# Kernel tuning notes

Measured on AMD Instinct MI355X. Metric: run time of the kernel, lower is better.

Reference implementation:

```python
import jax, jax.numpy as jnp
import numpy as np

B, S, D, H, W = 8, 2048, 128, 8, 64
INT_HEADS = 8          # hardcoded in SpatioTemporalLayer1
EPS_COS = 1e-8
EPS_LN = 1e-5


def _mha(q_in, k_in, v_in, in_w, in_b, out_w, out_b, nh, mask=None):
    # q_in/k_in/v_in: (batch, len, d); torch nn.MultiheadAttention math (eval, no dropout)
    b, lq, d = q_in.shape
    hd = d // nh
    q = (q_in @ in_w[:d].T + in_b[:d]).reshape(b, lq, nh, hd)
    k = (k_in @ in_w[d:2 * d].T + in_b[d:2 * d]).reshape(b, k_in.shape[1], nh, hd)
    v = (v_in @ in_w[2 * d:].T + in_b[2 * d:]).reshape(b, v_in.shape[1], nh, hd)
    scores = jnp.einsum('bihd,bjhd->bhij', q, k) / jnp.sqrt(jnp.asarray(hd, q_in.dtype))
    if mask is not None:
        scores = scores + mask
    attn = jax.nn.softmax(scores, axis=-1)
    out = jnp.einsum('bhij,bjhd->bihd', attn, v).reshape(b, lq, d)
    return out @ out_w.T + out_b


def _layernorm(x, g, b):
    mu = x.mean(-1, keepdims=True)
    var = ((x - mu) ** 2).mean(-1, keepdims=True)
    return (x - mu) * jax.lax.rsqrt(var + EPS_LN) * g + b


def _cos_normalize(e):
    n = jnp.maximum(jnp.linalg.norm(e, axis=-1, keepdims=True), EPS_COS)
    return e / n


def _forward(x, spatial_info, temporal_info,
             lw_in_w, lw_in_b, lw_out_w, lw_out_b,
             spat_w, spat_b, temp_w, temp_b,
             int_in_w, int_in_b, int_out_w, int_out_b,
             ffn_w1, ffn_b1, ffn_w2, ffn_b2,
             ln1_g, ln1_b, ln2_g, ln2_b):
    b, s, d = x.shape
    # --- local window attention (S % W == 0 here, so no padding path) ---
    nw = s // W
    xw = x.reshape(b * nw, W, d)
    causal = jnp.triu(jnp.full((W, W), -jnp.inf, x.dtype), k=1)
    attn = _mha(xw, xw, xw, lw_in_w, lw_in_b, lw_out_w, lw_out_b, H, causal).reshape(b, s, d)
    x = _layernorm(attn + x, ln1_g, ln1_b)
    # --- FFN (torch nn.GELU default = exact erf) ---
    h = jax.nn.gelu(x @ ffn_w1.T + ffn_b1, approximate=False)
    x = _layernorm(h @ ffn_w2.T + ffn_b2 + x, ln2_g, ln2_b)
    # --- spatio-temporal interaction ---
    se = spatial_info @ spat_w.T + spat_b
    te = temporal_info @ temp_w.T + temp_b
    sn = _cos_normalize(se)
    tn = _cos_normalize(te)
    ss = jnp.einsum('bid,bjd->bij', sn, sn)   # (B,S,S) spatial cosine sim
    ts = jnp.einsum('bid,bjd->bij', tn, tn)   # (B,S,S) temporal cosine sim
    # interaction MHA is batch_first=False: it treats (B,S,D) as (len=B, batch=S, d).
    # Equivalent batch-first call on swapped axes (faithful to the torch source).
    inter = jnp.swapaxes(
        _mha(jnp.swapaxes(se, 0, 1), jnp.swapaxes(te, 0, 1), jnp.swapaxes(te, 0, 1),
             int_in_w, int_in_b, int_out_w, int_out_b, INT_HEADS), 0, 1)
    # similarity[b,i,j,d] = ss[b,i,j]*ts[b,i,j]*inter[b,i,d]; mean over j factorizes:
    sim = (ss * ts).mean(axis=2)              # (B,S)
    return x + sim[..., None] * inter


def setup_inputs() -> dict:
    key = jax.random.key(0)
    ks = jax.random.split(key, 24)
    sc = 0.02
    inp = {
        'x': jax.random.normal(ks[0], (B, S, D), jnp.float32),
        'spatial_info': jax.random.normal(ks[1], (B, S, D), jnp.float32),
        'temporal_info': jax.random.normal(ks[2], (B, S, D), jnp.float32),
        'lw_in_w': jax.random.normal(ks[3], (3 * D, D), jnp.float32) * sc,
        'lw_in_b': jnp.zeros((3 * D,), jnp.float32),
        'lw_out_w': jax.random.normal(ks[4], (D, D), jnp.float32) * sc,
        'lw_out_b': jnp.zeros((D,), jnp.float32),
        'spat_w': jax.random.normal(ks[5], (D, D), jnp.float32) * sc,
        'spat_b': jnp.zeros((D,), jnp.float32),
        'temp_w': jax.random.normal(ks[6], (D, D), jnp.float32) * sc,
        'temp_b': jnp.zeros((D,), jnp.float32),
        'int_in_w': jax.random.normal(ks[7], (3 * D, D), jnp.float32) * sc,
        'int_in_b': jnp.zeros((3 * D,), jnp.float32),
        'int_out_w': jax.random.normal(ks[8], (D, D), jnp.float32) * sc,
        'int_out_b': jnp.zeros((D,), jnp.float32),
        'ffn_w1': jax.random.normal(ks[9], (4 * D, D), jnp.float32) * sc,
        'ffn_b1': jnp.zeros((4 * D,), jnp.float32),
        'ffn_w2': jax.random.normal(ks[10], (D, 4 * D), jnp.float32) * sc,
        'ffn_b2': jnp.zeros((D,), jnp.float32),
        'ln1_g': jnp.ones((D,), jnp.float32),
        'ln1_b': jnp.zeros((D,), jnp.float32),
        'ln2_g': jnp.ones((D,), jnp.float32),
        'ln2_b': jnp.zeros((D,), jnp.float32),
    }
    return inp


def reference(x, spatial_info, temporal_info,
              lw_in_w, lw_in_b, lw_out_w, lw_out_b,
              spat_w, spat_b, temp_w, temp_b,
              int_in_w, int_in_b, int_out_w, int_out_b,
              ffn_w1, ffn_b1, ffn_w2, ffn_b2,
              ln1_g, ln1_b, ln2_g, ln2_b):
    return _forward(x, spatial_info, temporal_info,
                    lw_in_w, lw_in_b, lw_out_w, lw_out_b,
                    spat_w, spat_b, temp_w, temp_b,
                    int_in_w, int_in_b, int_out_w, int_out_b,
                    ffn_w1, ffn_b1, ffn_w2, ffn_b2,
                    ln1_g, ln1_b, ln2_g, ln2_b)
```

## Files before the change

### kernel.cpp

```cpp
#include <hip/hip_runtime.h>
#include <math.h>

#define BB 8
#define SS 2048
#define NTOK (BB * SS)
#define ATB_SPLIT 16

using bf16x8 = __attribute__((ext_vector_type(8))) short;
using f32x4  = __attribute__((ext_vector_type(4))) float;

__device__ __forceinline__ float gelu_tanh(float x) {
    float y = 0.7978845608f * (x + 0.044715f * x * x * x);
    float e = __expf(2.0f * y);
    float t = 1.0f - 2.0f / (e + 1.0f);
    return 0.5f * x * (1.0f + t);
}
__device__ __forceinline__ unsigned short f2b(float f) {
    unsigned int u = __float_as_uint(f);
    u += 0x7FFFu + ((u >> 16) & 1u);
    return (unsigned short)(u >> 16);
}
__device__ __forceinline__ float b2f(unsigned short u) {
    return __uint_as_float((unsigned int)u << 16);
}
__device__ __forceinline__ bf16x8 ldg_f32_b8(const float* p) {
    float4 f0 = *(const float4*)p, f1 = *(const float4*)(p + 4);
    union { ushort4 u[2]; bf16x8 v; } r;
    r.u[0] = (ushort4){f2b(f0.x), f2b(f0.y), f2b(f0.z), f2b(f0.w)};
    r.u[1] = (ushort4){f2b(f1.x), f2b(f1.y), f2b(f1.z), f2b(f1.w)};
    return r.v;
}

__global__ __launch_bounds__(256) void phase1(
    const float* __restrict__ x,
    const float* __restrict__ lw_in_w, const float* __restrict__ b_in,
    const float* __restrict__ lw_out_w, const float* __restrict__ b_out,
    const float* __restrict__ lng, const float* __restrict__ lnb,
    float* __restrict__ x1, unsigned short* __restrict__ x1b,
    const float* __restrict__ ffn_w1, const float* __restrict__ ffn_w2,
    unsigned short* __restrict__ Wb,
    const float* __restrict__ spatial, const float* __restrict__ temporal,
    const float* __restrict__ spat_w, const float* __restrict__ temp_w,
    const float* __restrict__ bsp, const float* __restrict__ btp,
    unsigned short* __restrict__ snb, unsigned short* __restrict__ tnb,
    unsigned short* __restrict__ seb, unsigned short* __restrict__ teb)
{
    __shared__ unsigned short Qs[64 * 136];
    __shared__ unsigned short Ks[64 * 136];
    __shared__ unsigned short Vt[128 * 72];
    __shared__ unsigned short Pb[4][32 * 72];
    __shared__ float red[2][64][2];
    const int tid = threadIdx.x;
    const int wv = tid >> 6, lane = tid & 63, ln = lane & 15, q = lane >> 4;

    if (blockIdx.x >= 768) {
        const int idx2 = blockIdx.x - 768;
        const int y = idx2 >> 8;
        const int m0 = (idx2 & 255) * 64;
        const float* Af = y ? temporal : spatial;
        const float* Wf = y ? temp_w : spat_w;
        const float* bias = y ? btp : bsp;
        unsigned short* nb = y ? tnb : snb;
        unsigned short* raw = y ? teb : seb;
        const int wm = (wv >> 1) * 32, wn = (wv & 1) * 64;

        f32x4 acc[2][4] = {};
        #pragma unroll
        for (int kf = 0; kf < 4; ++kf) {
            bf16x8 a[2], b[4];
            #pragma unroll
            for (int fm = 0; fm < 2; ++fm)
                a[fm] = ldg_f32_b8(Af + (size_t)(m0 + wm + fm * 16 + ln) * 128 + kf * 32 + q * 8);
            #pragma unroll
            for (int fn = 0; fn < 4; ++fn)
                b[fn] = ldg_f32_b8(Wf + (size_t)(wn + fn * 16 + ln) * 128 + kf * 32 + q * 8);
            #pragma unroll
            for (int fm = 0; fm < 2; ++fm)
                #pragma unroll
                for (int fn = 0; fn < 4; ++fn)
                    acc[fm][fn] = __builtin_amdgcn_mfma_f32_16x16x32_bf16(a[fm], b[fn], acc[fm][fn], 0, 0, 0);
        }
        #pragma unroll
        for (int fm = 0; fm < 2; ++fm)
            #pragma unroll
            for (int r = 0; r < 4; ++r) {
                int rl = wm + fm * 16 + q * 4 + r;
                float s2 = 0.0f;
                #pragma unroll
                for (int fn = 0; fn < 4; ++fn) {
                    int col = wn + fn * 16 + ln;
                    float vv = acc[fm][fn][r] + bias[col];
                    acc[fm][fn][r] = vv;
                    s2 += vv * vv;
                }
                #pragma unroll
                for (int off = 1; off < 16; off <<= 1) s2 += __shfl_xor(s2, off, 64);
                if (ln == 0) red[0][rl][wv & 1] = s2;
            }
        __syncthreads();
        #pragma unroll
        for (int fm = 0; fm < 2; ++fm)
            #pragma unroll
            for (int r = 0; r < 4; ++r) {
                int rl = wm + fm * 16 + q * 4 + r;
                int row = m0 + rl;
                float inv = 1.0f / fmaxf(sqrtf(red[0][rl][0] + red[0][rl][1]), 1e-8f);
                #pragma unroll
                for (int fn = 0; fn < 4; ++fn) {
                    int col = wn + fn * 16 + ln;
                    float vv = acc[fm][fn][r];
                    nb[(size_t)row * 128 + col] = f2b(vv * inv);
                    raw[(size_t)row * 128 + col] = f2b(vv);
                }
            }
        return;
    }

    if (blockIdx.x >= 256) {
        int i = (blockIdx.x - 256) * 256 + tid;
        float v = (i < 65536) ? ffn_w1[i] : ffn_w2[i - 65536];
        Wb[i] = f2b(v);
        return;
    }

    const int m0 = blockIdx.x * 64;
    const int wm = (wv >> 1) * 32, wn = (wv & 1) * 64;

    bf16x8 afr[4][2];
    #pragma unroll
    for (int kf = 0; kf < 4; ++kf)
        #pragma unroll
        for (int fm = 0; fm < 2; ++fm)
            afr[kf][fm] = ldg_f32_b8(x + (size_t)(m0 + wm + fm * 16 + ln) * 128 + kf * 32 + q * 8);

    #pragma unroll
    for (int p = 0; p < 3; ++p) {
        f32x4 acc[2][4] = {};
        #pragma unroll
        for (int kf = 0; kf < 4; ++kf) {
            bf16x8 b[4];
            #pragma unroll
            for (int fn = 0; fn < 4; ++fn)
                b[fn] = ldg_f32_b8(lw_in_w + (size_t)(p * 128 + wn + fn * 16 + ln) * 128 + kf * 32 + q * 8);
            #pragma unroll
            for (int fm = 0; fm < 2; ++fm)
                #pragma unroll
                for (int fn = 0; fn < 4; ++fn)
                    acc[fm][fn] = __builtin_amdgcn_mfma_f32_16x16x32_bf16(afr[kf][fm], b[fn], acc[fm][fn], 0, 0, 0);
        }
        #pragma unroll
        for (int fm = 0; fm < 2; ++fm)
            #pragma unroll
            for (int r = 0; r < 4; ++r) {
                int rl = wm + fm * 16 + q * 4 + r;
                #pragma unroll
                for (int fn = 0; fn < 4; ++fn) {
                    int col = wn + fn * 16 + ln;
                    unsigned short v = f2b(acc[fm][fn][r] + b_in[p * 128 + col]);
                    if (p == 0)      Qs[rl * 136 + col] = v;
                    else if (p == 1) Ks[rl * 136 + col] = v;
                    else             Vt[col * 72 + rl] = v;
                }
            }
    }
    __syncthreads();

    {
        const int mh = wv >> 1, hq = wv & 1;
        unsigned short* P = &Pb[wv][0];
        #pragma unroll
        for (int hh = 0; hh < 4; ++hh) {
            const int h = hq * 4 + hh;
            f32x4 sacc[2][4] = {};
            bf16x8 az[2] = {}, bz[4] = {};
            if (q < 2) {
                #pragma unroll
                for (int fm = 0; fm < 2; ++fm)
                    az[fm] = *(const bf16x8*)&Qs[(mh * 32 + fm * 16 + ln) * 136 + h * 16 + q * 8];
                #pragma unroll
                for (int fn = 0; fn < 4; ++fn)
                    bz[fn] = *(const bf16x8*)&Ks[(fn * 16 + ln) * 136 + h * 16 + q * 8];
            }
            #pragma unroll
            for (int fm = 0; fm < 2; ++fm)
                #pragma unroll
                for (int fn = 0; fn < 4; ++fn)
                    sacc[fm][fn] = __builtin_amdgcn_mfma_f32_16x16x32_bf16(az[fm], bz[fn], sacc[fm][fn], 0, 0, 0);
            float invr[2][4];
            #pragma unroll
            for (int fm = 0; fm < 2; ++fm)
                #pragma unroll
                for (int r = 0; r < 4; ++r) {
                    int gi = mh * 32 + fm * 16 + q * 4 + r;
                    float mx = -1e30f;
                    #pragma unroll
                    for (int fn = 0; fn < 4; ++fn) {
                        int j = fn * 16 + ln;
                        float s = sacc[fm][fn][r] * 0.25f;
                        if (j > gi) s = -1e30f;
                        sacc[fm][fn][r] = s;
                        mx = fmaxf(mx, s);
                    }
                    #pragma unroll
                    for (int off = 1; off < 16; off <<= 1)
                        mx = fmaxf(mx, __shfl_xor(mx, off, 64));
                    float sum = 0.0f;
                    #pragma unroll
                    for (int fn = 0; fn < 4; ++fn) {
                        float p_ = __expf(sacc[fm][fn][r] - mx);
                        sacc[fm][fn][r] = p_;
                        sum += p_;
                    }
                    #pragma unroll
                    for (int off = 1; off < 16; off <<= 1)
                        sum += __shfl_xor(sum, off, 64);
                    invr[fm][r] = 1.0f / sum;
                    #pragma unroll
                    for (int fn = 0; fn < 4; ++fn)
                        P[(fm * 16 + q * 4 + r) * 72 + fn * 16 + ln] = f2b(sacc[fm][fn][r]);
                }
            f32x4 oacc[2] = {};
            #pragma unroll
            for (int kf2 = 0; kf2 < 2; ++kf2) {
                bf16x8 pa[2], vb;
                #pragma unroll
                for (int fm = 0; fm < 2; ++fm)
                    pa[fm] = *(const bf16x8*)&P[(fm * 16 + ln) * 72 + kf2 * 32 + q * 8];
                vb = *(const bf16x8*)&Vt[(h * 16 + ln) * 72 + kf2 * 32 + q * 8];
                #pragma unroll
                for (int fm = 0; fm < 2; ++fm)
                    oacc[fm] = __builtin_amdgcn_mfma_f32_16x16x32_bf16(pa[fm], vb, oacc[fm], 0, 0, 0);
            }
            #pragma unroll
            for (int fm = 0; fm < 2; ++fm)
                #pragma unroll
                for (int r = 0; r < 4; ++r)
                    Qs[(mh * 32 + fm * 16 + q * 4 + r) * 136 + h * 16 + ln] =
                        f2b(oacc[fm][r] * invr[fm][r]);
        }
    }
    __syncthreads();

    f32x4 acc[2][4] = {};
    #pragma unroll
    for (int kf = 0; kf < 4; ++kf) {
        bf16x8 a[2], b[4];
        #pragma unroll
        for (int fm = 0; fm < 2; ++fm)
            a[fm] = *(const bf16x8*)&Qs[(wm + fm * 16 + ln) * 136 + kf * 32 + q * 8];
        #pragma unroll
        for (int fn = 0; fn < 4; ++fn)
            b[fn] = ldg_f32_b8(lw_out_w + (size_t)(wn + fn * 16 + ln) * 128 + kf * 32 + q * 8);
        #pragma unroll
        for (int fm = 0; fm < 2; ++fm)
            #pragma unroll
            for (int fn = 0; fn < 4; ++fn)
                acc[fm][fn] = __builtin_amdgcn_mfma_f32_16x16x32_bf16(a[fm], b[fn], acc[fm][fn], 0, 0, 0);
    }
    #pragma unroll
    for (int fm = 0; fm < 2; ++fm)
        #pragma unroll
        for (int r = 0; r < 4; ++r) {
            int rl = wm + fm * 16 + q * 4 + r;
            int row = m0 + rl;
            float s1 = 0.0f, s2 = 0.0f;
            #pragma unroll
            for (int fn = 0; fn < 4; ++fn) {
                int col = wn + fn * 16 + ln;
                float vv = acc[fm][fn][r] + b_out[col] + x[(size_t)row * 128 + col];
                acc[fm][fn][r] = vv;
                s1 += vv; s2 += vv * vv;
            }
            #pragma unroll
            for (int off = 1; off < 16; off <<= 1) {
                s1 += __shfl_xor(s1, off, 64);
                s2 += __shfl_xor(s2, off, 64);
            }
            if (ln == 0) { red[0][rl][wv & 1] = s1; red[1][rl][wv & 1] = s2; }
        }
    __syncthreads();
    #pragma unroll
    for (int fm = 0; fm < 2; ++fm)
        #pragma unroll
        for (int r = 0; r < 4; ++r) {
            int rl = wm + fm * 16 + q * 4 + r;
            int row = m0 + rl;
            float mu = (red[0][rl][0] + red[0][rl][1]) * (1.0f / 128.0f);
            float var = (red[1][rl][0] + red[1][rl][1]) * (1.0f / 128.0f) - mu * mu;
            float rs = rsqrtf(var + 1e-5f);
            #pragma unroll
            for (int fn = 0; fn < 4; ++fn) {
                int col = wn + fn * 16 + ln;
                float o = (acc[fm][fn][r] - mu) * rs * lng[col] + lnb[col];
                x1[(size_t)row * 128 + col] = o;
                x1b[(size_t)row * 128 + col] = f2b(o);
            }
        }
}

__global__ __launch_bounds__(256) void phase2(
    const unsigned short* __restrict__ x1b, const float* __restrict__ x1,
    const unsigned short* __restrict__ Wb,
    const float* __restrict__ b1, const float* __restrict__ b2,
    const float* __restrict__ lng, const float* __restrict__ lnb,
    float* __restrict__ x2,
    const unsigned short* __restrict__ snb, const unsigned short* __restrict__ tnb,
    float* __restrict__ part)
{
    __shared__ __align__(16) char pool[36864];
    __shared__ float red[2][64][2];
    const int tid = threadIdx.x;
    const int wv = tid >> 6, lane = tid & 63, ln = lane & 15, q = lane >> 4;

    if (blockIdx.x < 256) {
        unsigned short* Xs = (unsigned short*)pool;
        unsigned short* Hs0 = (unsigned short*)(pool + 17408);
        unsigned short* Hs1 = (unsigned short*)(pool + 26624);
        const int t0 = blockIdx.x * 64;
        const int wm = (wv >> 1) * 32;
        const int wn1 = (wv & 1) * 32, wn2 = (wv & 1) * 64;
        const unsigned short* w1 = Wb;
        const unsigned short* w2 = Wb + 65536;

        const uint4* X4 = (const uint4*)(x1b + (size_t)t0 * 128);
        #pragma unroll
        for (int t = 0; t < 4; ++t) {
            int idx = tid + t * 256;
            int r = idx >> 4, c = idx & 15;
            *(uint4*)&Xs[r * 136 + c * 8] = X4[r * 16 + c];
        }
        __syncthreads();

        f32x4 acc2[2][4] = {};
        for (int ch = 0; ch < 8; ++ch) {
            const int hc0 = ch * 64;
            unsigned short* Hb = (ch & 1) ? Hs1 : Hs0;
            f32x4 acc1[2][2] = {};
            #pragma unroll
            for (int kf = 0; kf < 4; ++kf) {
                bf16x8 a[2], b[2];
                #pragma unroll
                for (int fm = 0; fm < 2; ++fm)
                    a[fm] = *(const bf16x8*)&Xs[(wm + fm * 16 + ln) * 136 + kf * 32 + q * 8];
                #pragma unroll
                for (int fn = 0; fn < 2; ++fn)
                    b[fn] = *(const bf16x8*)&w1[(size_t)(hc0 + wn1 + fn * 16 + ln) * 128 + kf * 32 + q * 8];
                #pragma unroll
                for (int fm = 0; fm < 2; ++fm)
                    #pragma unroll
                    for (int fn = 0; fn < 2; ++fn)
                        acc1[fm][fn] = __builtin_amdgcn_mfma_f32_16x16x32_bf16(a[fm], b[fn], acc1[fm][fn], 0, 0, 0);
            }
            #pragma unroll
            for (int fm = 0; fm < 2; ++fm)
                #pragma unroll
                for (int fn = 0; fn < 2; ++fn)
                    #pragma unroll
                    for (int r = 0; r < 4; ++r) {
                        int rl = wm + fm * 16 + q * 4 + r;
                        int col = wn1 + fn * 16 + ln;
                        Hb[rl * 72 + col] = f2b(gelu_tanh(acc1[fm][fn][r] + b1[hc0 + col]));
                    }
            __syncthreads();
            #pragma unroll
            for (int kf2 = 0; kf2 < 2; ++kf2) {
                bf16x8 a[2], b[4];
                #pragma unroll
                for (int fm = 0; fm < 2; ++fm)
                    a[fm] = *(const bf16x8*)&Hb[(wm + fm * 16 + ln) * 72 + kf2 * 32 + q * 8];
                #pragma unroll
                for (int fn = 0; fn < 4; ++fn)
                    b[fn] = *(const bf16x8*)&w2[(size_t)(wn2 + fn * 16 + ln) * 512 + hc0 + kf2 * 32 + q * 8];
                #pragma unroll
                for (int fm = 0; fm < 2; ++fm)
                    #pragma unroll
                    for (int fn = 0; fn < 4; ++fn)
                        acc2[fm][fn] = __builtin_amdgcn_mfma_f32_16x16x32_bf16(a[fm], b[fn], acc2[fm][fn], 0, 0, 0);
            }
        }
        #pragma unroll
        for (int fm = 0; fm < 2; ++fm)
            #pragma unroll
            for (int r = 0; r < 4; ++r) {
                int rl = wm + fm * 16 + q * 4 + r;
                int row = t0 + rl;
                float s1 = 0.0f, s2 = 0.0f;
                #pragma unroll
                for (int fn = 0; fn < 4; ++fn) {
                    int col = wn2 + fn * 16 + ln;
                    float vv = acc2[fm][fn][r] + b2[col] + x1[(size_t)row * 128 + col];
                    acc2[fm][fn][r] = vv;
                    s1 += vv; s2 += vv * vv;
                }
                #pragma unroll
                for (int off = 1; off < 16; off <<= 1) {
                    s1 += __shfl_xor(s1, off, 64);
                    s2 += __shfl_xor(s2, off, 64);
                }
                if (ln == 0) { red[0][rl][wv & 1] = s1; red[1][rl][wv & 1] = s2; }
            }
        __syncthreads();
        #pragma unroll
        for (int fm = 0; fm < 2; ++fm)
            #pragma unroll
            for (int r = 0; r < 4; ++r) {
                int rl = wm + fm * 16 + q * 4 + r;
                int row = t0 + rl;
                float mu = (red[0][rl][0] + red[0][rl][1]) * (1.0f / 128.0f);
                float var = (red[1][rl][0] + red[1][rl][1]) * (1.0f / 128.0f) - mu * mu;
                float rs = rsqrtf(var + 1e-5f);
                #pragma unroll
                for (int fn = 0; fn < 4; ++fn) {
                    int col = wn2 + fn * 16 + ln;
                    x2[(size_t)row * 128 + col] = (acc2[fm][fn][r] - mu) * rs * lng[col] + lnb[col];
                }
            }
        return;
    }

    {
        unsigned short* Sst = (unsigned short*)pool;
        unsigned short* Tst = (unsigned short*)(pool + 17408);
        const int idx2 = blockIdx.x - 256;
        const int d0 = (idx2 & 1) * 64, e0 = ((idx2 >> 1) & 1) * 64;
        const int z = idx2 >> 2;
        const int b = z >> 4, chunk = z & 15;
        const size_t rowb = (size_t)(b * SS + chunk * 128);

        #pragma unroll
        for (int it = 0; it < 4; ++it) {
            int j = (tid & 31) + it * 32;
            int c8 = (tid >> 5) * 8;
            uint4 sv = *(const uint4*)&snb[(rowb + j) * 128 + d0 + c8];
            uint4 tv = *(const uint4*)&tnb[(rowb + j) * 128 + e0 + c8];
            const unsigned short* sp = (const unsigned short*)&sv;
            const unsigned short* tp = (const unsigned short*)&tv;
            #pragma unroll
            for (int c = 0; c < 8; ++c) {
                Sst[(c8 + c) * 136 + j] = sp[c];
                Tst[(c8 + c) * 136 + j] = tp[c];
            }
        }
        __syncthreads();

        const int wm = (wv >> 1) * 32, wn = (wv & 1) * 32;
        f32x4 acc[2][2] = {};
        #pragma unroll
        for (int kf = 0; kf < 4; ++kf) {
            bf16x8 a[2], bb[2];
            #pragma unroll
            for (int fm = 0; fm < 2; ++fm)
                a[fm] = *(const bf16x8*)&Sst[(wm + fm * 16 + ln) * 136 + kf * 32 + q * 8];
            #pragma unroll
            for (int fn = 0; fn < 2; ++fn)
                bb[fn] = *(const bf16x8*)&Tst[(wn + fn * 16 + ln) * 136 + kf * 32 + q * 8];
            #pragma unroll
            for (int fm = 0; fm < 2; ++fm)
                #pragma unroll
                for (int fn = 0; fn < 2; ++fn)
                    acc[fm][fn] = __builtin_amdgcn_mfma_f32_16x16x32_bf16(a[fm], bb[fn], acc[fm][fn], 0, 0, 0);
        }
        float* pp = part + (size_t)(b * ATB_SPLIT + chunk) * 16384;
        #pragma unroll
        for (int fm = 0; fm < 2; ++fm)
            #pragma unroll
            for (int r = 0; r < 4; ++r) {
                int dd = d0 + wm + fm * 16 + q * 4 + r;
                #pragma unroll
                for (int fn = 0; fn < 2; ++fn) {
                    int ee = e0 + wn + fn * 16 + ln;
                    pp[(size_t)dd * 128 + ee] = acc[fm][fn][r];
                }
            }
    }
}

__global__ __launch_bounds__(256) void atb_reduce_kernel(
    const float* __restrict__ part, unsigned short* __restrict__ Mtb)
{
    int i = blockIdx.x * 256 + threadIdx.x;
    int b = i >> 14, rem = i & 16383;
    int e = rem >> 7, d = rem & 127;
    const float* pp = part + (size_t)b * ATB_SPLIT * 16384 + (size_t)d * 128 + e;
    float s = 0.0f;
    #pragma unroll
    for (int c = 0; c < ATB_SPLIT; ++c) s += pp[(size_t)c * 16384];
    Mtb[i] = f2b(s);
}

__global__ __launch_bounds__(256) void simgemm_kernel(
    const unsigned short* __restrict__ snb, const unsigned short* __restrict__ tnb,
    const unsigned short* __restrict__ Mtb, float* __restrict__ sim)
{
    __shared__ float red[64][2];
    const int tid = threadIdx.x, m0 = blockIdx.x * 64, b = m0 >> 11;
    const int wv = tid >> 6, lane = tid & 63, ln = lane & 15, q = lane >> 4;
    const int wm = (wv >> 1) * 32, wn = (wv & 1) * 64;

    f32x4 acc[2][4] = {};
    #pragma unroll
    for (int kf = 0; kf < 4; ++kf) {
        bf16x8 a[2], bb[4];
        #pragma unroll
        for (int fm = 0; fm < 2; ++fm)
            a[fm] = *(const bf16x8*)&snb[(size_t)(m0 + wm + fm * 16 + ln) * 128 + kf * 32 + q * 8];
        #pragma unroll
        for (int fn = 0; fn < 4; ++fn)
            bb[fn] = *(const bf16x8*)&Mtb[(size_t)b * 16384 + (size_t)(wn + fn * 16 + ln) * 128 + kf * 32 + q * 8];
        #pragma unroll
        for (int fm = 0; fm < 2; ++fm)
            #pragma unroll
            for (int fn = 0; fn < 4; ++fn)
                acc[fm][fn] = __builtin_amdgcn_mfma_f32_16x16x32_bf16(a[fm], bb[fn], acc[fm][fn], 0, 0, 0);
    }
    #pragma unroll
    for (int fm = 0; fm < 2; ++fm)
        #pragma unroll
        for (int r = 0; r < 4; ++r) {
            int rl = wm + fm * 16 + q * 4 + r;
            int row = m0 + rl;
            float s = 0.0f;
            #pragma unroll
            for (int fn = 0; fn < 4; ++fn) {
                int col = wn + fn * 16 + ln;
                s += acc[fm][fn][r] * b2f(tnb[(size_t)row * 128 + col]);
            }
            #pragma unroll
            for (int off = 1; off < 16; off <<= 1) s += __shfl_xor(s, off, 64);
            if (ln == 0) red[rl][wv & 1] = s;
        }
    __syncthreads();
    if (tid < 64) sim[m0 + tid] = (red[tid][0] + red[tid][1]) * (1.0f / (float)SS);
}

__global__ __launch_bounds__(256) void inter_block(
    const unsigned short* __restrict__ seb, const unsigned short* __restrict__ teb,
    const float* __restrict__ Wint,
    const float* __restrict__ b_int,
    const float* __restrict__ Wio,
    const float* __restrict__ b_io,
    const float* __restrict__ sim, const float* __restrict__ x2,
    float* __restrict__ out)
{
    __shared__ unsigned short Qs[64 * 136];
    __shared__ unsigned short KVs[64 * 256];
    const int tid = threadIdx.x, s0 = blockIdx.x * 8;
    const int wv = tid >> 6, lane = tid & 63, ln = lane & 15, q = lane >> 4;
    const int wm = (wv >> 1) * 32, wn = (wv & 1) * 64;

    bf16x8 afr[4][2];
    #pragma unroll
    for (int kf = 0; kf < 4; ++kf)
        #pragma unroll
        for (int fm = 0; fm < 2; ++fm) {
            int rl = wm + fm * 16 + ln;
            size_t g = (size_t)(rl >> 3) * 2048 + s0 + (rl & 7);
            afr[kf][fm] = *(const bf16x8*)&seb[g * 128 + kf * 32 + q * 8];
        }

    #pragma unroll
    for (int p = 0; p < 3; ++p) {
        if (p == 1) {
            #pragma unroll
            for (int kf = 0; kf < 4; ++kf)
                #pragma unroll
                for (int fm = 0; fm < 2; ++fm) {
                    int rl = wm + fm * 16 + ln;
                    size_t g = (size_t)(rl >> 3) * 2048 + s0 + (rl & 7);
                    afr[kf][fm] = *(const bf16x8*)&teb[g * 128 + kf * 32 + q * 8];
                }
        }
        f32x4 acc[2][4] = {};
        #pragma unroll
        for (int kf = 0; kf < 4; ++kf) {
            bf16x8 b[4];
            #pragma unroll
            for (int fn = 0; fn < 4; ++fn)
                b[fn] = ldg_f32_b8(Wint + (size_t)(p * 128 + wn + fn * 16 + ln) * 128 + kf * 32 + q * 8);
            #pragma unroll
            for (int fm = 0; fm < 2; ++fm)
                #pragma unroll
                for (int fn = 0; fn < 4; ++fn)
                    acc[fm][fn] = __builtin_amdgcn_mfma_f32_16x16x32_bf16(afr[kf][fm], b[fn], acc[fm][fn], 0, 0, 0);
        }
        #pragma unroll
        for (int fm = 0; fm < 2; ++fm)
            #pragma unroll
            for (int r = 0; r < 4; ++r) {
                int rl = wm + fm * 16 + q * 4 + r;
                #pragma unroll
                for (int fn = 0; fn < 4; ++fn) {
                    int col = wn + fn * 16 + ln;
                    unsigned short v = f2b(acc[fm][fn][r] + b_int[p * 128 + col]);
                    if (p == 0) Qs[rl * 136 + col] = v;
                    else        KVs[rl * 256 + (p - 1) * 128 + col] = v;
                }
            }
        __syncthreads();
    }

    #pragma unroll
    for (int tt = 0; tt < 2; ++tt) {
        int task = tid + tt * 256;
        int ss = task >> 6, h = (task >> 3) & 7, i = task & 7;
        int rq = i * 8 + ss;
        float qr[16];
        {
            uint4 q0 = *(const uint4*)&Qs[rq * 136 + h * 16];
            uint4 q1 = *(const uint4*)&Qs[rq * 136 + h * 16 + 8];
            const unsigned short* p0 = (const unsigned short*)&q0;
            const unsigned short* p1 = (const unsigned short*)&q1;
            #pragma unroll
            for (int c = 0; c < 8; ++c) { qr[c] = b2f(p0[c]); qr[8 + c] = b2f(p1[c]); }
        }
        float sc[8];
        #pragma unroll
        for (int j = 0; j < 8; ++j) {
            uint4 k0 = *(const uint4*)&KVs[(j * 8 + ss) * 256 + h * 16];
            uint4 k1 = *(const uint4*)&KVs[(j * 8 + ss) * 256 + h * 16 + 8];
            const unsigned short* kp0 = (const unsigned short*)&k0;
            const unsigned short* kp1 = (const unsigned short*)&k1;
            float s = 0.0f;
            #pragma unroll
            for (int c = 0; c < 8; ++c) {
                s = fmaf(qr[c], b2f(kp0[c]), s);
                s = fmaf(qr[8 + c], b2f(kp1[c]), s);
            }
            sc[j] = s * 0.25f;
        }
        float mx = -1e30f;
        #pragma unroll
        for (int j = 0; j < 8; ++j) mx = fmaxf(mx, sc[j]);
        float pe[8], se = 0.0f;
        #pragma unroll
        for (int j = 0; j < 8; ++j) { pe[j] = __expf(sc[j] - mx); se += pe[j]; }
        float inv = 1.0f / se;
        float o[16] = {};
        #pragma unroll
        for (int j = 0; j < 8; ++j) {
            uint4 v0 = *(const uint4*)&KVs[(j * 8 + ss) * 256 + 128 + h * 16];
            uint4 v1 = *(const uint4*)&KVs[(j * 8 + ss) * 256 + 128 + h * 16 + 8];
            const unsigned short* vp0 = (const unsigned short*)&v0;
            const unsigned short* vp1 = (const unsigned short*)&v1;
            #pragma unroll
            for (int c = 0; c < 8; ++c) {
                o[c]     += pe[j] * b2f(vp0[c]);
                o[8 + c] += pe[j] * b2f(vp1[c]);
            }
        }
        ushort4 w0 = (ushort4){f2b(o[0]*inv),  f2b(o[1]*inv),  f2b(o[2]*inv),  f2b(o[3]*inv)};
        ushort4 w1 = (ushort4){f2b(o[4]*inv),  f2b(o[5]*inv),  f2b(o[6]*inv),  f2b(o[7]*inv)};
        ushort4 w2 = (ushort4){f2b(o[8]*inv),  f2b(o[9]*inv),  f2b(o[10]*inv), f2b(o[11]*inv)};
        ushort4 w3 = (ushort4){f2b(o[12]*inv), f2b(o[13]*inv), f2b(o[14]*inv), f2b(o[15]*inv)};
        *(ushort4*)&Qs[rq * 136 + h * 16]      = w0;
        *(ushort4*)&Qs[rq * 136 + h * 16 + 4]  = w1;
        *(ushort4*)&Qs[rq * 136 + h * 16 + 8]  = w2;
        *(ushort4*)&Qs[rq * 136 + h * 16 + 12] = w3;
    }
    __syncthreads();

    f32x4 acc[2][4] = {};
    #pragma unroll
    for (int kf = 0; kf < 4; ++kf) {
        bf16x8 a[2], b[4];
        #pragma unroll
        for (int fm = 0; fm < 2; ++fm)
            a[fm] = *(const bf16x8*)&Qs[(wm + fm * 16 + ln) * 136 + kf * 32 + q * 8];
        #pragma unroll
        for (int fn = 0; fn < 4; ++fn)
            b[fn] = ldg_f32_b8(Wio + (size_t)(wn + fn * 16 + ln) * 128 + kf * 32 + q * 8);
        #pragma unroll
        for (int fm = 0; fm < 2; ++fm)
            #pragma unroll
            for (int fn = 0; fn < 4; ++fn)
                acc[fm][fn] = __builtin_amdgcn_mfma_f32_16x16x32_bf16(a[fm], b[fn], acc[fm][fn], 0, 0, 0);
    }
    #pragma unroll
    for (int fm = 0; fm < 2; ++fm)
        #pragma unroll
        for (int r = 0; r < 4; ++r) {
            int rl = wm + fm * 16 + q * 4 + r;
            size_t g = (size_t)(rl >> 3) * 2048 + s0 + (rl & 7);
            float sc = sim[g];
            #pragma unroll
            for (int fn = 0; fn < 4; ++fn) {
                int col = wn + fn * 16 + ln;
                out[g * 128 + col] = (acc[fm][fn][r] + b_io[col]) * sc + x2[g * 128 + col];
            }
        }
}

extern "C" void kernel_launch(void* const* d_in, const int* in_sizes, int n_in,
                              void* d_out, int out_size, void* d_ws, size_t ws_size,
                              hipStream_t stream)
{
    const float* x        = (const float*)d_in[0];
    const float* spatial  = (const float*)d_in[1];
    const float* temporal = (const float*)d_in[2];
    const float* lw_in_w  = (const float*)d_in[3];
    const float* lw_in_b  = (const float*)d_in[4];
    const float* lw_out_w = (const float*)d_in[5];
    const float* lw_out_b = (const float*)d_in[6];
    const float* spat_w   = (const float*)d_in[7];
    const float* spat_b   = (const float*)d_in[8];
    const float* temp_w   = (const float*)d_in[9];
    const float* temp_b   = (const float*)d_in[10];
    const float* int_in_w = (const float*)d_in[11];
    const float* int_in_b = (const float*)d_in[12];
    const float* int_out_w= (const float*)d_in[13];
    const float* int_out_b= (const float*)d_in[14];
    const float* ffn_b1   = (const float*)d_in[16];
    const float* ffn_b2   = (const float*)d_in[18];
    const float* ln1_g    = (const float*)d_in[19];
    const float* ln1_b    = (const float*)d_in[20];
    const float* ln2_g    = (const float*)d_in[21];
    const float* ln2_b    = (const float*)d_in[22];
    float* out = (float*)d_out;

    char* base = (char*)d_ws;
    float*          x1   = (float*)(base + 0);
    unsigned short* x1b  = (unsigned short*)(base + 8388608);
    float*          x2   = (float*)(base + 12582912);
    unsigned short* snb  = (unsigned short*)(base + 20971520);
    unsigned short* tnb  = (unsigned short*)(base + 25165824);
    unsigned short* seb  = (unsigned short*)(base + 29360128);
    unsigned short* teb  = (unsigned short*)(base + 33554432);
    unsigned short* Mtb  = (unsigned short*)(base + 37748736);
    float*          simb = (float*)(base + 38010880);
    unsigned short* Wb   = (unsigned short*)(base + 38076416);
    float*          part = (float*)(base + 38338560);

    phase1<<<1280, 256, 0, stream>>>(
        x, lw_in_w, lw_in_b, lw_out_w, lw_out_b, ln1_g, ln1_b, x1, x1b,
        (const float*)d_in[15], (const float*)d_in[17], Wb,
        spatial, temporal, spat_w, temp_w, spat_b, temp_b,
        snb, tnb, seb, teb);
    phase2<<<768, 256, 0, stream>>>(
        x1b, x1, Wb, ffn_b1, ffn_b2, ln2_g, ln2_b, x2, snb, tnb, part);
    atb_reduce_kernel<<<512, 256, 0, stream>>>(part, Mtb);
    simgemm_kernel<<<256, 256, 0, stream>>>(snb, tnb, Mtb, simb);
    inter_block<<<256, 256, 0, stream>>>(
        seb, teb, int_in_w, int_in_b, int_out_w, int_out_b, simb, x2, out);
}
```

Baseline: 235.1 us.

## Replace split-K partials and reduce kernel with atomic accumulation; pre-convert interaction weights to bf16

Phase2's T^T·S partial products are now accumulated directly into a zeroed fp32 matrix with atomic adds, which removes the separate reduction kernel, the partial-buffer traffic and one launch. Phase1's conversion blocks now use vectorized float4 loads to convert the FFN and interaction weights to bf16 and to zero the accumulator, so inter_block reads bf16 weights directly. Launch bounds with occupancy hints are added to several kernels. The atomics make the summation order nondeterministic and can contend on shared addresses, and simgemm now converts the fp32 matrix to bf16 on load.

```diff
diff --git a/kernel.cpp b/kernel.cpp
--- a/kernel.cpp
+++ b/kernel.cpp
@@ -4,7 +4,6 @@
 #define BB 8
 #define SS 2048
 #define NTOK (BB * SS)
-#define ATB_SPLIT 16
 
 using bf16x8 = __attribute__((ext_vector_type(8))) short;
 using f32x4  = __attribute__((ext_vector_type(4))) float;
@@ -31,7 +30,7 @@
     return r.v;
 }
 
-__global__ __launch_bounds__(256) void phase1(
+__global__ __launch_bounds__(256, 2) void phase1(
     const float* __restrict__ x,
     const float* __restrict__ lw_in_w, const float* __restrict__ b_in,
     const float* __restrict__ lw_out_w, const float* __restrict__ b_out,
@@ -39,6 +38,9 @@
     float* __restrict__ x1, unsigned short* __restrict__ x1b,
     const float* __restrict__ ffn_w1, const float* __restrict__ ffn_w2,
     unsigned short* __restrict__ Wb,
+    const float* __restrict__ int_in_w, const float* __restrict__ int_out_w,
+    unsigned short* __restrict__ Wib, unsigned short* __restrict__ Wiob,
+    float* __restrict__ Mf,
     const float* __restrict__ spatial, const float* __restrict__ temporal,
     const float* __restrict__ spat_w, const float* __restrict__ temp_w,
     const float* __restrict__ bsp, const float* __restrict__ btp,
@@ -53,8 +55,8 @@
     const int tid = threadIdx.x;
     const int wv = tid >> 6, lane = tid & 63, ln = lane & 15, q = lane >> 4;
 
-    if (blockIdx.x >= 768) {
-        const int idx2 = blockIdx.x - 768;
+    if (blockIdx.x >= 320) {
+        const int idx2 = blockIdx.x - 320;
         const int y = idx2 >> 8;
         const int m0 = (idx2 & 255) * 64;
         const float* Af = y ? temporal : spatial;
@@ -117,9 +119,24 @@
     }
 
     if (blockIdx.x >= 256) {
-        int i = (blockIdx.x - 256) * 256 + tid;
-        float v = (i < 65536) ? ffn_w1[i] : ffn_w2[i - 65536];
-        Wb[i] = f2b(v);
+        int gt = (blockIdx.x - 256) * 256 + tid;
+        #pragma unroll
+        for (int s = 0; s < 3; ++s) {
+            int v = gt + s * 16384;
+            const float* src;
+            unsigned short* dst;
+            int off;
+            if (v < 16384)      { src = ffn_w1;   dst = Wb;         off = v; }
+            else if (v < 32768) { src = ffn_w2;   dst = Wb + 65536; off = v - 16384; }
+            else if (v < 45056) { src = int_in_w; dst = Wib;        off = v - 32768; }
+            else                { src = int_out_w; dst = Wiob;      off = v - 45056; }
+            float4 f = *(const float4*)(src + (size_t)off * 4);
+            *(ushort4*)(dst + (size_t)off * 4) =
+                (ushort4){f2b(f.x), f2b(f.y), f2b(f.z), f2b(f.w)};
+        }
+        float4 z4 = (float4){0.f, 0.f, 0.f, 0.f};
+        *(float4*)(Mf + (size_t)gt * 4) = z4;
+        *(float4*)(Mf + (size_t)(gt + 16384) * 4) = z4;
         return;
     }
 
@@ -298,14 +315,14 @@
         }
 }
 
-__global__ __launch_bounds__(256) void phase2(
+__global__ __launch_bounds__(256, 4) void phase2(
     const unsigned short* __restrict__ x1b, const float* __restrict__ x1,
     const unsigned short* __restrict__ Wb,
     const float* __restrict__ b1, const float* __restrict__ b2,
     const float* __restrict__ lng, const float* __restrict__ lnb,
     float* __restrict__ x2,
     const unsigned short* __restrict__ snb, const unsigned short* __restrict__ tnb,
-    float* __restrict__ part)
+    float* __restrict__ Mf)
 {
     __shared__ __align__(16) char pool[36864];
     __shared__ float red[2][64][2];
@@ -450,47 +467,34 @@
             bf16x8 a[2], bb[2];
             #pragma unroll
             for (int fm = 0; fm < 2; ++fm)
-                a[fm] = *(const bf16x8*)&Sst[(wm + fm * 16 + ln) * 136 + kf * 32 + q * 8];
+                a[fm] = *(const bf16x8*)&Tst[(wm + fm * 16 + ln) * 136 + kf * 32 + q * 8];
             #pragma unroll
             for (int fn = 0; fn < 2; ++fn)
-                bb[fn] = *(const bf16x8*)&Tst[(wn + fn * 16 + ln) * 136 + kf * 32 + q * 8];
+                bb[fn] = *(const bf16x8*)&Sst[(wn + fn * 16 + ln) * 136 + kf * 32 + q * 8];
             #pragma unroll
             for (int fm = 0; fm < 2; ++fm)
                 #pragma unroll
                 for (int fn = 0; fn < 2; ++fn)
                     acc[fm][fn] = __builtin_amdgcn_mfma_f32_16x16x32_bf16(a[fm], bb[fn], acc[fm][fn], 0, 0, 0);
         }
-        float* pp = part + (size_t)(b * ATB_SPLIT + chunk) * 16384;
+        float* pp = Mf + (size_t)b * 16384;
         #pragma unroll
         for (int fm = 0; fm < 2; ++fm)
             #pragma unroll
             for (int r = 0; r < 4; ++r) {
-                int dd = d0 + wm + fm * 16 + q * 4 + r;
+                int ee = e0 + wm + fm * 16 + q * 4 + r;
                 #pragma unroll
                 for (int fn = 0; fn < 2; ++fn) {
-                    int ee = e0 + wn + fn * 16 + ln;
-                    pp[(size_t)dd * 128 + ee] = acc[fm][fn][r];
-                }
-            }
-    }
-}
-
-__global__ __launch_bounds__(256) void atb_reduce_kernel(
-    const float* __restrict__ part, unsigned short* __restrict__ Mtb)
-{
-    int i = blockIdx.x * 256 + threadIdx.x;
-    int b = i >> 14, rem = i & 16383;
-    int e = rem >> 7, d = rem & 127;
-    const float* pp = part + (size_t)b * ATB_SPLIT * 16384 + (size_t)d * 128 + e;
-    float s = 0.0f;
-    #pragma unroll
-    for (int c = 0; c < ATB_SPLIT; ++c) s += pp[(size_t)c * 16384];
-    Mtb[i] = f2b(s);
-}
-
-__global__ __launch_bounds__(256) void simgemm_kernel(
+                    int dd = d0 + wn + fn * 16 + ln;
+                    unsafeAtomicAdd(&pp[(size_t)ee * 128 + dd], acc[fm][fn][r]);
+                }
+            }
+    }
+}
+
+__global__ __launch_bounds__(256, 1) void simgemm_kernel(
     const unsigned short* __restrict__ snb, const unsigned short* __restrict__ tnb,
-    const unsigned short* __restrict__ Mtb, float* __restrict__ sim)
+    const float* __restrict__ Mf, float* __restrict__ sim)
 {
     __shared__ float red[64][2];
     const int tid = threadIdx.x, m0 = blockIdx.x * 64, b = m0 >> 11;
@@ -506,7 +510,7 @@
             a[fm] = *(const bf16x8*)&snb[(size_t)(m0 + wm + fm * 16 + ln) * 128 + kf * 32 + q * 8];
         #pragma unroll
         for (int fn = 0; fn < 4; ++fn)
-            bb[fn] = *(const bf16x8*)&Mtb[(size_t)b * 16384 + (size_t)(wn + fn * 16 + ln) * 128 + kf * 32 + q * 8];
+            bb[fn] = ldg_f32_b8(Mf + (size_t)b * 16384 + (size_t)(wn + fn * 16 + ln) * 128 + kf * 32 + q * 8);
         #pragma unroll
         for (int fm = 0; fm < 2; ++fm)
             #pragma unroll
@@ -533,11 +537,11 @@
     if (tid < 64) sim[m0 + tid] = (red[tid][0] + red[tid][1]) * (1.0f / (float)SS);
 }
 
-__global__ __launch_bounds__(256) void inter_block(
+__global__ __launch_bounds__(256, 3) void inter_block(
     const unsigned short* __restrict__ seb, const unsigned short* __restrict__ teb,
-    const float* __restrict__ Wint,
+    const unsigned short* __restrict__ Wib,
     const float* __restrict__ b_int,
-    const float* __restrict__ Wio,
+    const unsigned short* __restrict__ Wiob,
     const float* __restrict__ b_io,
     const float* __restrict__ sim, const float* __restrict__ x2,
     float* __restrict__ out)
@@ -576,7 +580,7 @@
             bf16x8 b[4];
             #pragma unroll
             for (int fn = 0; fn < 4; ++fn)
-                b[fn] = ldg_f32_b8(Wint + (size_t)(p * 128 + wn + fn * 16 + ln) * 128 + kf * 32 + q * 8);
+                b[fn] = *(const bf16x8*)&Wib[(size_t)(p * 128 + wn + fn * 16 + ln) * 128 + kf * 32 + q * 8];
             #pragma unroll
             for (int fm = 0; fm < 2; ++fm)
                 #pragma unroll
@@ -668,7 +672,7 @@
             a[fm] = *(const bf16x8*)&Qs[(wm + fm * 16 + ln) * 136 + kf * 32 + q * 8];
         #pragma unroll
         for (int fn = 0; fn < 4; ++fn)
-            b[fn] = ldg_f32_b8(Wio + (size_t)(wn + fn * 16 + ln) * 128 + kf * 32 + q * 8);
+            b[fn] = *(const bf16x8*)&Wiob[(size_t)(wn + fn * 16 + ln) * 128 + kf * 32 + q * 8];
         #pragma unroll
         for (int fm = 0; fm < 2; ++fm)
             #pragma unroll
@@ -725,20 +729,21 @@
     unsigned short* tnb  = (unsigned short*)(base + 25165824);
     unsigned short* seb  = (unsigned short*)(base + 29360128);
     unsigned short* teb  = (unsigned short*)(base + 33554432);
-    unsigned short* Mtb  = (unsigned short*)(base + 37748736);
-    float*          simb = (float*)(base + 38010880);
-    unsigned short* Wb   = (unsigned short*)(base + 38076416);
-    float*          part = (float*)(base + 38338560);
-
-    phase1<<<1280, 256, 0, stream>>>(
+    unsigned short* Wb   = (unsigned short*)(base + 37748736);
+    unsigned short* Wib  = (unsigned short*)(base + 38010880);
+    unsigned short* Wiob = (unsigned short*)(base + 38109184);
+    float*          Mf   = (float*)(base + 38141952);
+    float*          simb = (float*)(base + 38666240);
+
+    phase1<<<832, 256, 0, stream>>>(
         x, lw_in_w, lw_in_b, lw_out_w, lw_out_b, ln1_g, ln1_b, x1, x1b,
         (const float*)d_in[15], (const float*)d_in[17], Wb,
+        int_in_w, int_out_w, Wib, Wiob, Mf,
         spatial, temporal, spat_w, temp_w, spat_b, temp_b,
         snb, tnb, seb, teb);
     phase2<<<768, 256, 0, stream>>>(
-        x1b, x1, Wb, ffn_b1, ffn_b2, ln2_g, ln2_b, x2, snb, tnb, part);
-    atb_reduce_kernel<<<512, 256, 0, stream>>>(part, Mtb);
-    simgemm_kernel<<<256, 256, 0, stream>>>(snb, tnb, Mtb, simb);
+        x1b, x1, Wb, ffn_b1, ffn_b2, ln2_g, ln2_b, x2, snb, tnb, Mf);
+    simgemm_kernel<<<256, 256, 0, stream>>>(snb, tnb, Mf, simb);
     inter_block<<<256, 256, 0, stream>>>(
-        seb, teb, int_in_w, int_in_b, int_out_w, int_out_b, simb, x2, out);
-}
+        seb, teb, Wib, int_in_b, Wiob, int_out_b, simb, x2, out);
+}
```

New measurement: 271.1 us. 1.15x slower.
